# Performance work log

Measured on AMD Instinct MI355X. Metric: run time of the kernel, lower is better.

Reference implementation:

```python
import jax, jax.numpy as jnp
import numpy as np
import math
from jax import lax


def _conv1d(x, w, stride=1):
    """Cross-correlation (torch F.conv1d semantics), VALID. x:[B,L], w:[K] -> [B,Lout]."""
    out = lax.conv_general_dilated(
        x[:, None, :], w[None, None, :], window_strides=(stride,), padding='VALID',
        dimension_numbers=('NCH', 'OIH', 'NCH'))
    return out[:, 0, :]


def setup_inputs() -> dict:
    B, D, K, NS = 32768, 1024, 8, 10  # batch, dim, filter_length, num_sparse_params
    key = jax.random.key(0)
    k_x, k_lo, k_hi, k_sp = jax.random.split(key, 4)
    x = jax.random.normal(k_x, (B, D), dtype=jnp.float32)
    sqrt2 = math.sqrt(2.0)
    base_lo = jnp.array([1.0, 1.0], dtype=jnp.float32) / sqrt2
    base_hi = jnp.array([1.0, -1.0], dtype=jnp.float32) / sqrt2
    dec_lo = jnp.pad(base_lo, (0, K - 2)) + 0.01 * jax.random.normal(k_lo, (K,), jnp.float32)
    dec_hi = jnp.pad(base_hi, (0, K - 2)) + 0.01 * jax.random.normal(k_hi, (K,), jnp.float32)
    rec_lo = dec_lo  # cloned from dec at init
    rec_hi = dec_hi
    std = math.sqrt(2.0 / D)
    sparse_coeffs = std * jax.random.normal(k_sp, (NS,), jnp.float32)
    # distinct indices from randperm(dim), all < 2*coeff_len so all valid
    sparse_indices = jnp.asarray(np.random.default_rng(0).permutation(D)[:NS], dtype=jnp.int32)
    return {"x": x, "dec_lo": dec_lo, "dec_hi": dec_hi, "rec_lo": rec_lo,
            "rec_hi": rec_hi, "sparse_coeffs": sparse_coeffs,
            "sparse_indices": sparse_indices}


def reference(x, dec_lo, dec_hi, rec_lo, rec_hi, sparse_coeffs, sparse_indices):
    B, D = x.shape
    K = dec_lo.shape[0]
    p = K - 1  # reflect pad size = 7
    # ---- DWT: reflect pad, correlate with flipped dec filters, stride-2 downsample ----
    xp = jnp.pad(x, ((0, 0), (p, p)), mode='reflect')          # [B, D+14]
    lo = _conv1d(xp, dec_lo[::-1], stride=2)                   # [B, 516]
    hi = _conv1d(xp, dec_hi[::-1], stride=2)                   # [B, 516]
    Lc = lo.shape[1]
    # ---- sparse coefficient injection at fixed indices (distinct indices) ----
    flat = jnp.concatenate([lo, hi], axis=1)                   # [B, 2*Lc]
    flat = flat.at[:, sparse_indices].add(sparse_coeffs[None, :])
    lo2, hi2 = flat[:, :Lc], flat[:, Lc:2 * Lc]
    # ---- IDWT: zero-upsample, reflect pad, correlate with rec filters ----
    up_lo = jnp.zeros((B, 2 * Lc), x.dtype).at[:, ::2].set(lo2)
    up_hi = jnp.zeros((B, 2 * Lc), x.dtype).at[:, ::2].set(hi2)
    up_lo = jnp.pad(up_lo, ((0, 0), (p, p)), mode='reflect')
    up_hi = jnp.pad(up_hi, ((0, 0), (p, p)), mode='reflect')
    rec = _conv1d(up_lo, rec_lo) + _conv1d(up_hi, rec_hi)      # [B, 2*Lc + p] = [B, 1039]
    rec = rec[:, :D]                                           # crop to target length (1039 > 1024)
    return x + rec
```

## Files before the change

### kernel.cpp

```cpp
#include <hip/hip_runtime.h>

#define D_LEN 1024
#define K_LEN 8
#define NS    10
#define LCC   516
#define GRID  2048

__global__ __launch_bounds__(256) void wavecore_kernel(
    const float* __restrict__ x,
    const float* __restrict__ dec_lo, const float* __restrict__ dec_hi,
    const float* __restrict__ rec_lo, const float* __restrict__ rec_hi,
    const float* __restrict__ sp_c,   const int* __restrict__ sp_i,
    float* __restrict__ out, int J)
{
    __shared__ __align__(16) float  sx[2][D_LEN];
    __shared__ __align__(16) float2 st[2][512];

    const int tid = threadIdx.x;

    float fdl[K_LEN], fdh[K_LEN], frl[K_LEN], frh[K_LEN];
#pragma unroll
    for (int k = 0; k < K_LEN; ++k) {
        fdl[k] = dec_lo[k]; fdh[k] = dec_hi[k];
        frl[k] = rec_lo[k]; frh[k] = rec_hi[k];
    }

    float dq0, dq1, dq2, dq3;
    {
        float4 z; z.x = 0.f; z.y = 0.f; z.z = 0.f; z.w = 0.f;
        ((float4*)st[0])[tid] = z;
        __syncthreads();
        if (tid < NS) {
            const int   s = sp_i[tid];
            const float v = sp_c[tid];
            if (s < 512)       st[0][s].x = v;
            else if (s >= LCC) st[0][s - LCC].y = v;
        }
        __syncthreads();
        if (tid >= 2) {
            const float4 qa = ((const float4*)st[0])[tid - 2];
            const float4 qb = ((const float4*)st[0])[tid - 1];
            const float4 qc = ((const float4*)st[0])[tid];
            const float p0l = qa.z, p0h = qa.w;
            const float p1l = qb.x, p1h = qb.y;
            const float p2l = qb.z, p2h = qb.w;
            const float p3l = qc.x, p3h = qc.y;
            const float p4l = qc.z, p4h = qc.w;
            dq0 = p0l*frl[1] + p0h*frh[1] + p1l*frl[3] + p1h*frh[3]
                + p2l*frl[5] + p2h*frh[5] + p3l*frl[7] + p3h*frh[7];
            dq1 = p0l*frl[0] + p0h*frh[0] + p1l*frl[2] + p1h*frh[2]
                + p2l*frl[4] + p2h*frh[4] + p3l*frl[6] + p3h*frh[6];
            dq2 = p1l*frl[1] + p1h*frh[1] + p2l*frl[3] + p2h*frh[3]
                + p3l*frl[5] + p3h*frh[5] + p4l*frl[7] + p4h*frh[7];
            dq3 = p1l*frl[0] + p1h*frh[0] + p2l*frl[2] + p2h*frh[2]
                + p3l*frl[4] + p3h*frh[4] + p4l*frl[6] + p4h*frh[6];
        } else {
            float acc[4];
#pragma unroll
            for (int j = 0; j < 4; ++j) {
                const int t  = 4 * tid + j;
                const int k0 = ((j & 1) ^ 1);
                float a = 0.f;
#pragma unroll
                for (int i = 0; i < 4; ++i) {
                    const int k = k0 + 2 * i;
                    int m = t + k - 7;
                    m = (m < 0) ? -m : m;
                    const float2 pv = st[0][m >> 1];
                    a = fmaf(pv.x, frl[k], a);
                    a = fmaf(pv.y, frh[k], a);
                }
                acc[j] = a;
            }
            dq0 = acc[0]; dq1 = acc[1]; dq2 = acc[2]; dq3 = acc[3];
        }
        __syncthreads();
    }

    size_t off = (size_t)blockIdx.x * D_LEN + 4 * (size_t)tid;
    const size_t rstride = (size_t)GRID * D_LEN;
    float4 xv = *(const float4*)(x + off);
    ((float4*)sx[0])[tid] = xv;
    float4 xn = *(const float4*)(x + off + rstride);
    __syncthreads();

    int cur = 0, sb = 0;
#pragma unroll 1
    for (int j = 0; j < J; ++j) {
        float4 xn2;
        if (j + 2 < J) xn2 = *(const float4*)(x + off + 2 * rstride);

        const float* sxc = sx[cur];
        float lo0 = 0.f, hi0 = 0.f, lo1 = 0.f, hi1 = 0.f;
        if (tid >= 2) {
            const float4 wa = ((const float4*)sxc)[tid - 2];
            const float4 wb = ((const float4*)sxc)[tid - 1];
            const float w[12] = { wa.x, wa.y, wa.z, wa.w,
                                  wb.x, wb.y, wb.z, wb.w,
                                  xv.x, xv.y, xv.z, xv.w };
#pragma unroll
            for (int jj = 0; jj < K_LEN; ++jj) {
                const float v0 = w[8  - jj];
                const float v1 = w[10 - jj];
                lo0 = fmaf(v0, fdl[jj], lo0);
                hi0 = fmaf(v0, fdh[jj], hi0);
                lo1 = fmaf(v1, fdl[jj], lo1);
                hi1 = fmaf(v1, fdh[jj], hi1);
            }
        } else {
#pragma unroll
            for (int q = 0; q < 2; ++q) {
                const int c = 2 * tid + q;
                float aL = 0.f, aH = 0.f;
#pragma unroll
                for (int jj = 0; jj < K_LEN; ++jj) {
                    int m = 2 * c - jj;
                    m = (m < 0) ? -m : m;
                    const float v = sxc[m];
                    aL = fmaf(v, fdl[jj], aL);
                    aH = fmaf(v, fdh[jj], aH);
                }
                if (q == 0) { lo0 = aL; hi0 = aH; }
                else        { lo1 = aL; hi1 = aH; }
            }
        }
        {
            float4 pr; pr.x = lo0; pr.y = hi0; pr.z = lo1; pr.w = hi1;
            ((float4*)st[sb])[tid] = pr;
        }
        if (j + 1 < J) ((float4*)sx[cur ^ 1])[tid] = xn;
        __syncthreads();

        float res0, res1, res2, res3;
        if (tid >= 2) {
            const float4 qa = ((const float4*)st[sb])[tid - 2];
            const float4 qb = ((const float4*)st[sb])[tid - 1];
            const float p0l = qa.z, p0h = qa.w;
            const float p1l = qb.x, p1h = qb.y;
            const float p2l = qb.z, p2h = qb.w;
            const float p3l = lo0,  p3h = hi0;
            const float p4l = lo1,  p4h = hi1;
            res0 = p0l*frl[1] + p0h*frh[1] + p1l*frl[3] + p1h*frh[3]
                 + p2l*frl[5] + p2h*frh[5] + p3l*frl[7] + p3h*frh[7];
            res1 = p0l*frl[0] + p0h*frh[0] + p1l*frl[2] + p1h*frh[2]
                 + p2l*frl[4] + p2h*frh[4] + p3l*frl[6] + p3h*frh[6];
            res2 = p1l*frl[1] + p1h*frh[1] + p2l*frl[3] + p2h*frh[3]
                 + p3l*frl[5] + p3h*frh[5] + p4l*frl[7] + p4h*frh[7];
            res3 = p1l*frl[0] + p1h*frh[0] + p2l*frl[2] + p2h*frh[2]
                 + p3l*frl[4] + p3h*frh[4] + p4l*frl[6] + p4h*frh[6];
        } else {
            float acc[4];
#pragma unroll
            for (int jj = 0; jj < 4; ++jj) {
                const int t  = 4 * tid + jj;
                const int k0 = ((jj & 1) ^ 1);
                float a = 0.f;
#pragma unroll
                for (int i = 0; i < 4; ++i) {
                    const int k = k0 + 2 * i;
                    int m = t + k - 7;
                    m = (m < 0) ? -m : m;
                    const float2 pv = st[sb][m >> 1];
                    a = fmaf(pv.x, frl[k], a);
                    a = fmaf(pv.y, frh[k], a);
                }
                acc[jj] = a;
            }
            res0 = acc[0]; res1 = acc[1]; res2 = acc[2]; res3 = acc[3];
        }

        float4 r;
        r.x = res0 + xv.x + dq0;
        r.y = res1 + xv.y + dq1;
        r.z = res2 + xv.z + dq2;
        r.w = res3 + xv.w + dq3;
        *(float4*)(out + off) = r;

        xv = xn; xn = xn2; cur ^= 1; sb ^= 1; off += rstride;
    }
}

extern "C" void kernel_launch(void* const* d_in, const int* in_sizes, int n_in,
                              void* d_out, int out_size, void* d_ws, size_t ws_size,
                              hipStream_t stream) {
    const float* x      = (const float*)d_in[0];
    const float* dec_lo = (const float*)d_in[1];
    const float* dec_hi = (const float*)d_in[2];
    const float* rec_lo = (const float*)d_in[3];
    const float* rec_hi = (const float*)d_in[4];
    const float* sp_c   = (const float*)d_in[5];
    const int*   sp_i   = (const int*)d_in[6];
    float* out = (float*)d_out;

    const int Brows = in_sizes[0] / D_LEN;
    const int J     = Brows / GRID;

    wavecore_kernel<<<GRID, 256, 0, stream>>>(x, dec_lo, dec_hi, rec_lo, rec_hi,
                                              sp_c, sp_i, out, J);
}
```

Measured before the change: 46.62 us.

## Process one row per wavefront to drop block-wide barriers in main loop

Restructures the kernel so each 64-lane wavefront owns a whole 1024-element row in its own LDS slice, with each lane handling four float4 segments. The main loop no longer needs __syncthreads, because the stage-to-stage data exchange stays within one wavefront. Rows are now contiguous per wave (4 rows each) and the grid becomes Brows/16 blocks. The change also uses more LDS (20KB) and more registers per thread, and it relies on wave-synchronous LDS ordering within a wavefront without any explicit barrier.

Result: slower. 48.55 us (+4.1%).

```diff
diff --git a/kernel.cpp b/kernel.cpp
--- a/kernel.cpp
+++ b/kernel.cpp
@@ -4,7 +4,6 @@
 #define K_LEN 8
 #define NS    10
 #define LCC   516
-#define GRID  2048
 
 __global__ __launch_bounds__(256) void wavecore_kernel(
     const float* __restrict__ x,
@@ -13,10 +12,13 @@
     const float* __restrict__ sp_c,   const int* __restrict__ sp_i,
     float* __restrict__ out, int J)
 {
-    __shared__ __align__(16) float  sx[2][D_LEN];
-    __shared__ __align__(16) float2 st[2][512];
+    __shared__ __align__(16) float lds[5 * D_LEN];
 
     const int tid = threadIdx.x;
+    const int l   = tid & 63;
+    const int w   = tid >> 6;
+    float* const dq  = lds;
+    float* const slc = lds + D_LEN * (1 + w);
 
     float fdl[K_LEN], fdh[K_LEN], frl[K_LEN], frh[K_LEN];
 #pragma unroll
@@ -25,158 +27,182 @@
         frl[k] = rec_lo[k]; frh[k] = rec_hi[k];
     }
 
-    float dq0, dq1, dq2, dq3;
-    {
+    if (w == 0) {
+        float2* const pr = (float2*)slc;
         float4 z; z.x = 0.f; z.y = 0.f; z.z = 0.f; z.w = 0.f;
-        ((float4*)st[0])[tid] = z;
-        __syncthreads();
-        if (tid < NS) {
-            const int   s = sp_i[tid];
-            const float v = sp_c[tid];
-            if (s < 512)       st[0][s].x = v;
-            else if (s >= LCC) st[0][s - LCC].y = v;
-        }
-        __syncthreads();
-        if (tid >= 2) {
-            const float4 qa = ((const float4*)st[0])[tid - 2];
-            const float4 qb = ((const float4*)st[0])[tid - 1];
-            const float4 qc = ((const float4*)st[0])[tid];
-            const float p0l = qa.z, p0h = qa.w;
-            const float p1l = qb.x, p1h = qb.y;
-            const float p2l = qb.z, p2h = qb.w;
-            const float p3l = qc.x, p3h = qc.y;
-            const float p4l = qc.z, p4h = qc.w;
-            dq0 = p0l*frl[1] + p0h*frh[1] + p1l*frl[3] + p1h*frh[3]
-                + p2l*frl[5] + p2h*frh[5] + p3l*frl[7] + p3h*frh[7];
-            dq1 = p0l*frl[0] + p0h*frh[0] + p1l*frl[2] + p1h*frh[2]
-                + p2l*frl[4] + p2h*frh[4] + p3l*frl[6] + p3h*frh[6];
-            dq2 = p1l*frl[1] + p1h*frh[1] + p2l*frl[3] + p2h*frh[3]
-                + p3l*frl[5] + p3h*frh[5] + p4l*frl[7] + p4h*frh[7];
-            dq3 = p1l*frl[0] + p1h*frh[0] + p2l*frl[2] + p2h*frh[2]
-                + p3l*frl[4] + p3h*frh[4] + p4l*frl[6] + p4h*frh[6];
-        } else {
-            float acc[4];
-#pragma unroll
-            for (int j = 0; j < 4; ++j) {
-                const int t  = 4 * tid + j;
-                const int k0 = ((j & 1) ^ 1);
-                float a = 0.f;
-#pragma unroll
-                for (int i = 0; i < 4; ++i) {
-                    const int k = k0 + 2 * i;
-                    int m = t + k - 7;
-                    m = (m < 0) ? -m : m;
-                    const float2 pv = st[0][m >> 1];
-                    a = fmaf(pv.x, frl[k], a);
-                    a = fmaf(pv.y, frh[k], a);
-                }
-                acc[j] = a;
+#pragma unroll
+        for (int s = 0; s < 4; ++s) ((float4*)pr)[64 * s + l] = z;
+        if (l < NS) {
+            const int   si = sp_i[l];
+            const float v  = sp_c[l];
+            if (si < 512)       pr[si].x       = v;
+            else if (si >= LCC) pr[si - LCC].y = v;
+        }
+#pragma unroll
+        for (int s = 0; s < 4; ++s) {
+            const int q = 64 * s + l;
+            float r0, r1, r2, r3;
+            if (q >= 2) {
+                const float4 qa = ((const float4*)pr)[q - 2];
+                const float4 qb = ((const float4*)pr)[q - 1];
+                const float4 qc = ((const float4*)pr)[q];
+                const float p0l = qa.z, p0h = qa.w;
+                const float p1l = qb.x, p1h = qb.y;
+                const float p2l = qb.z, p2h = qb.w;
+                const float p3l = qc.x, p3h = qc.y;
+                const float p4l = qc.z, p4h = qc.w;
+                r0 = p0l*frl[1] + p0h*frh[1] + p1l*frl[3] + p1h*frh[3]
+                   + p2l*frl[5] + p2h*frh[5] + p3l*frl[7] + p3h*frh[7];
+                r1 = p0l*frl[0] + p0h*frh[0] + p1l*frl[2] + p1h*frh[2]
+                   + p2l*frl[4] + p2h*frh[4] + p3l*frl[6] + p3h*frh[6];
+                r2 = p1l*frl[1] + p1h*frh[1] + p2l*frl[3] + p2h*frh[3]
+                   + p3l*frl[5] + p3h*frh[5] + p4l*frl[7] + p4h*frh[7];
+                r3 = p1l*frl[0] + p1h*frh[0] + p2l*frl[2] + p2h*frh[2]
+                   + p3l*frl[4] + p3h*frh[4] + p4l*frl[6] + p4h*frh[6];
+            } else {
+                float acc[4];
+#pragma unroll
+                for (int jj = 0; jj < 4; ++jj) {
+                    const int t  = 4 * q + jj;
+                    const int k0 = (t & 1) ? 0 : 1;
+                    float a = 0.f;
+#pragma unroll
+                    for (int u = 0; u < 4; ++u) {
+                        const int k = k0 + 2 * u;
+                        int m = t + k - 7;
+                        m = (m < 0) ? -m : m;
+                        const float2 pv = pr[m >> 1];
+                        a = fmaf(pv.x, frl[k], a);
+                        a = fmaf(pv.y, frh[k], a);
+                    }
+                    acc[jj] = a;
+                }
+                r0 = acc[0]; r1 = acc[1]; r2 = acc[2]; r3 = acc[3];
             }
-            dq0 = acc[0]; dq1 = acc[1]; dq2 = acc[2]; dq3 = acc[3];
-        }
-        __syncthreads();
+            float4 r; r.x = r0; r.y = r1; r.z = r2; r.w = r3;
+            ((float4*)dq)[q] = r;
+        }
     }
-
-    size_t off = (size_t)blockIdx.x * D_LEN + 4 * (size_t)tid;
-    const size_t rstride = (size_t)GRID * D_LEN;
-    float4 xv = *(const float4*)(x + off);
-    ((float4*)sx[0])[tid] = xv;
-    float4 xn = *(const float4*)(x + off + rstride);
     __syncthreads();
 
-    int cur = 0, sb = 0;
+    float4 dvq[4];
+#pragma unroll
+    for (int s = 0; s < 4; ++s) dvq[s] = ((const float4*)dq)[64 * s + l];
+
+    const int W = blockIdx.x * 4 + w;
+    const float* const xrow = x   + (size_t)W * J * D_LEN;
+    float*       const orow = out + (size_t)W * J * D_LEN;
+
+    float4 stg[4];
+#pragma unroll
+    for (int s = 0; s < 4; ++s) stg[s] = *(const float4*)(xrow + 4 * (64 * s + l));
+
 #pragma unroll 1
     for (int j = 0; j < J; ++j) {
-        float4 xn2;
-        if (j + 2 < J) xn2 = *(const float4*)(x + off + 2 * rstride);
-
-        const float* sxc = sx[cur];
-        float lo0 = 0.f, hi0 = 0.f, lo1 = 0.f, hi1 = 0.f;
-        if (tid >= 2) {
-            const float4 wa = ((const float4*)sxc)[tid - 2];
-            const float4 wb = ((const float4*)sxc)[tid - 1];
-            const float w[12] = { wa.x, wa.y, wa.z, wa.w,
-                                  wb.x, wb.y, wb.z, wb.w,
-                                  xv.x, xv.y, xv.z, xv.w };
-#pragma unroll
-            for (int jj = 0; jj < K_LEN; ++jj) {
-                const float v0 = w[8  - jj];
-                const float v1 = w[10 - jj];
-                lo0 = fmaf(v0, fdl[jj], lo0);
-                hi0 = fmaf(v0, fdh[jj], hi0);
-                lo1 = fmaf(v1, fdl[jj], lo1);
-                hi1 = fmaf(v1, fdh[jj], hi1);
+        float4 cur[4];
+#pragma unroll
+        for (int s = 0; s < 4; ++s) cur[s] = stg[s];
+#pragma unroll
+        for (int s = 0; s < 4; ++s) *(float4*)(slc + 4 * (64 * s + l)) = cur[s];
+        if (j + 1 < J) {
+            const float* const xn = xrow + (size_t)(j + 1) * D_LEN;
+#pragma unroll
+            for (int s = 0; s < 4; ++s) stg[s] = *(const float4*)(xn + 4 * (64 * s + l));
+        }
+
+        float4 P[4];
+#pragma unroll
+        for (int s = 0; s < 4; ++s) {
+            const int q = 64 * s + l;
+            float lo0 = 0.f, hi0 = 0.f, lo1 = 0.f, hi1 = 0.f;
+            if (s >= 1 || l >= 2) {
+                const float4 wa = *(const float4*)(slc + 4 * q - 8);
+                const float4 wb = *(const float4*)(slc + 4 * q - 4);
+                const float wv[12] = { wa.x, wa.y, wa.z, wa.w,
+                                       wb.x, wb.y, wb.z, wb.w,
+                                       cur[s].x, cur[s].y, cur[s].z, cur[s].w };
+#pragma unroll
+                for (int jj = 0; jj < K_LEN; ++jj) {
+                    const float v0 = wv[8  - jj];
+                    const float v1 = wv[10 - jj];
+                    lo0 = fmaf(v0, fdl[jj], lo0);
+                    hi0 = fmaf(v0, fdh[jj], hi0);
+                    lo1 = fmaf(v1, fdl[jj], lo1);
+                    hi1 = fmaf(v1, fdh[jj], hi1);
+                }
+            } else {
+#pragma unroll
+                for (int qq = 0; qq < 2; ++qq) {
+                    const int c = 2 * l + qq;
+                    float aL = 0.f, aH = 0.f;
+#pragma unroll
+                    for (int jj = 0; jj < K_LEN; ++jj) {
+                        int m = 2 * c - jj;
+                        m = (m < 0) ? -m : m;
+                        const float v = slc[m];
+                        aL = fmaf(v, fdl[jj], aL);
+                        aH = fmaf(v, fdh[jj], aH);
+                    }
+                    if (qq == 0) { lo0 = aL; hi0 = aH; }
+                    else         { lo1 = aL; hi1 = aH; }
+                }
             }
-        } else {
-#pragma unroll
-            for (int q = 0; q < 2; ++q) {
-                const int c = 2 * tid + q;
-                float aL = 0.f, aH = 0.f;
-#pragma unroll
-                for (int jj = 0; jj < K_LEN; ++jj) {
-                    int m = 2 * c - jj;
-                    m = (m < 0) ? -m : m;
-                    const float v = sxc[m];
-                    aL = fmaf(v, fdl[jj], aL);
-                    aH = fmaf(v, fdh[jj], aH);
-                }
-                if (q == 0) { lo0 = aL; hi0 = aH; }
-                else        { lo1 = aL; hi1 = aH; }
+            float4 p; p.x = lo0; p.y = hi0; p.z = lo1; p.w = hi1;
+            P[s] = p;
+        }
+
+#pragma unroll
+        for (int s = 0; s < 4; ++s) *(float4*)(slc + 4 * (64 * s + l)) = P[s];
+
+        float* const oj = orow + (size_t)j * D_LEN;
+#pragma unroll
+        for (int s = 0; s < 4; ++s) {
+            const int q = 64 * s + l;
+            float res0, res1, res2, res3;
+            if (s >= 1 || l >= 2) {
+                const float4 qa = *(const float4*)(slc + 4 * q - 8);
+                const float4 qb = *(const float4*)(slc + 4 * q - 4);
+                const float p0l = qa.z,   p0h = qa.w;
+                const float p1l = qb.x,   p1h = qb.y;
+                const float p2l = qb.z,   p2h = qb.w;
+                const float p3l = P[s].x, p3h = P[s].y;
+                const float p4l = P[s].z, p4h = P[s].w;
+                res0 = p0l*frl[1] + p0h*frh[1] + p1l*frl[3] + p1h*frh[3]
+                     + p2l*frl[5] + p2h*frh[5] + p3l*frl[7] + p3h*frh[7];
+                res1 = p0l*frl[0] + p0h*frh[0] + p1l*frl[2] + p1h*frh[2]
+                     + p2l*frl[4] + p2h*frh[4] + p3l*frl[6] + p3h*frh[6];
+                res2 = p1l*frl[1] + p1h*frh[1] + p2l*frl[3] + p2h*frh[3]
+                     + p3l*frl[5] + p3h*frh[5] + p4l*frl[7] + p4h*frh[7];
+                res3 = p1l*frl[0] + p1h*frh[0] + p2l*frl[2] + p2h*frh[2]
+                     + p3l*frl[4] + p3h*frh[4] + p4l*frl[6] + p4h*frh[6];
+            } else {
+                const float2* const prs = (const float2*)slc;
+                float acc[4];
+#pragma unroll
+                for (int jj = 0; jj < 4; ++jj) {
+                    const int t  = 4 * q + jj;
+                    const int k0 = (t & 1) ? 0 : 1;
+                    float a = 0.f;
+#pragma unroll
+                    for (int u = 0; u < 4; ++u) {
+                        const int k = k0 + 2 * u;
+                        int m = t + k - 7;
+                        m = (m < 0) ? -m : m;
+                        const float2 pv = prs[m >> 1];
+                        a = fmaf(pv.x, frl[k], a);
+                        a = fmaf(pv.y, frh[k], a);
+                    }
+                    acc[jj] = a;
+                }
+                res0 = acc[0]; res1 = acc[1]; res2 = acc[2]; res3 = acc[3];
             }
-        }
-        {
-            float4 pr; pr.x = lo0; pr.y = hi0; pr.z = lo1; pr.w = hi1;
-            ((float4*)st[sb])[tid] = pr;
-        }
-        if (j + 1 < J) ((float4*)sx[cur ^ 1])[tid] = xn;
-        __syncthreads();
-
-        float res0, res1, res2, res3;
-        if (tid >= 2) {
-            const float4 qa = ((const float4*)st[sb])[tid - 2];
-            const float4 qb = ((const float4*)st[sb])[tid - 1];
-            const float p0l = qa.z, p0h = qa.w;
-            const float p1l = qb.x, p1h = qb.y;
-            const float p2l = qb.z, p2h = qb.w;
-            const float p3l = lo0,  p3h = hi0;
-            const float p4l = lo1,  p4h = hi1;
-            res0 = p0l*frl[1] + p0h*frh[1] + p1l*frl[3] + p1h*frh[3]
-                 + p2l*frl[5] + p2h*frh[5] + p3l*frl[7] + p3h*frh[7];
-            res1 = p0l*frl[0] + p0h*frh[0] + p1l*frl[2] + p1h*frh[2]
-                 + p2l*frl[4] + p2h*frh[4] + p3l*frl[6] + p3h*frh[6];
-            res2 = p1l*frl[1] + p1h*frh[1] + p2l*frl[3] + p2h*frh[3]
-                 + p3l*frl[5] + p3h*frh[5] + p4l*frl[7] + p4h*frh[7];
-            res3 = p1l*frl[0] + p1h*frh[0] + p2l*frl[2] + p2h*frh[2]
-                 + p3l*frl[4] + p3h*frh[4] + p4l*frl[6] + p4h*frh[6];
-        } else {
-            float acc[4];
-#pragma unroll
-            for (int jj = 0; jj < 4; ++jj) {
-                const int t  = 4 * tid + jj;
-                const int k0 = ((jj & 1) ^ 1);
-                float a = 0.f;
-#pragma unroll
-                for (int i = 0; i < 4; ++i) {
-                    const int k = k0 + 2 * i;
-                    int m = t + k - 7;
-                    m = (m < 0) ? -m : m;
-                    const float2 pv = st[sb][m >> 1];
-                    a = fmaf(pv.x, frl[k], a);
-                    a = fmaf(pv.y, frh[k], a);
-                }
-                acc[jj] = a;
-            }
-            res0 = acc[0]; res1 = acc[1]; res2 = acc[2]; res3 = acc[3];
-        }
-
-        float4 r;
-        r.x = res0 + xv.x + dq0;
-        r.y = res1 + xv.y + dq1;
-        r.z = res2 + xv.z + dq2;
-        r.w = res3 + xv.w + dq3;
-        *(float4*)(out + off) = r;
-
-        xv = xn; xn = xn2; cur ^= 1; sb ^= 1; off += rstride;
+            float4 r;
+            r.x = res0 + cur[s].x + dvq[s].x;
+            r.y = res1 + cur[s].y + dvq[s].y;
+            r.z = res2 + cur[s].z + dvq[s].z;
+            r.w = res3 + cur[s].w + dvq[s].w;
+            *(float4*)(oj + 4 * q) = r;
+        }
     }
 }
 
@@ -192,9 +218,9 @@
     const int*   sp_i   = (const int*)d_in[6];
     float* out = (float*)d_out;
 
-    const int Brows = in_sizes[0] / D_LEN;
-    const int J     = Brows / GRID;
-
-    wavecore_kernel<<<GRID, 256, 0, stream>>>(x, dec_lo, dec_hi, rec_lo, rec_hi,
-                                              sp_c, sp_i, out, J);
+    const int Brows  = in_sizes[0] / D_LEN;
+    const int J      = 4;
+    const int blocks = Brows / (4 * J);
+    wavecore_kernel<<<blocks, 256, 0, stream>>>(x, dec_lo, dec_hi, rec_lo, rec_hi,
+                                                sp_c, sp_i, out, J);
 }
```
